# Kernel tuning notes

Measured on AMD Instinct MI355X. Metric: run time of the kernel, lower is better.

## Reference

```python
import jax, jax.numpy as jnp
import numpy as np

B, C, H, HEADS, WS, TOPK = 16, 112, 64, 4, 4, 128
NWH = H // WS          # 16 windows per side
NWIN = NWH * NWH       # 256 windows
HD = C // HEADS        # 28
SCALE = HD ** -0.5


def _topk_indices():
    # Geometric top-K closest full-res pixels per window center (level 0 of focal attention).
    f = H // NWH  # window stride on full-res grid
    qh = np.arange(NWH) * f + f // 2
    cq = np.stack(np.meshgrid(qh, qh, indexing='ij'), 0).reshape(2, -1)            # (2, NWIN)
    ck = np.stack(np.meshgrid(np.arange(H), np.arange(H), indexing='ij'), 0).reshape(2, -1)  # (2, H*H)
    d = np.sqrt(((cq[:, :, None].astype(np.float32) - ck[:, None, :]) ** 2).sum(0))
    return np.argsort(d, axis=1, kind='stable')[:, :TOPK].astype(np.int32)        # (NWIN, TOPK)


def setup_inputs() -> dict:
    key = jax.random.key(0)
    k1, k2, k3 = jax.random.split(key, 3)
    return {
        'x': jax.random.normal(k1, (B, C, H, H), jnp.float32),
        'Wqkv': jax.random.normal(k2, (3 * C, C), jnp.float32) * 0.02,
        'Wproj': jax.random.normal(k3, (C, C), jnp.float32) * 0.02,
        'bproj': jnp.zeros((C,), jnp.float32),
        'topk_idx': jnp.asarray(_topk_indices()),
    }


def reference(x, Wqkv, Wproj, bproj, topk_idx):
    Bv, Cv, Hv, Wv = x.shape
    nwin = (Hv // WS) * (Wv // WS)
    xt = jnp.transpose(x, (0, 2, 3, 1))                       # (B, H, W, C)
    qkv = jnp.einsum('bhwc,dc->bhwd', xt, Wqkv)               # 1x1 conv == matmul
    q, k, v = jnp.split(qkv, 3, axis=-1)
    # Window-partition queries: (B*nwin, heads, ws^2, hd)
    qw = q.reshape(Bv, Hv // WS, WS, Wv // WS, WS, Cv)
    qw = jnp.transpose(qw, (0, 1, 3, 2, 4, 5)).reshape(Bv * nwin, WS * WS, HEADS, HD)
    qw = jnp.transpose(qw, (0, 2, 1, 3)) * SCALE
    # Gather top-K K/V tokens per window from the full-resolution token list
    kf = k.reshape(Bv, Hv * Wv, HEADS, HD)
    vf = v.reshape(Bv, Hv * Wv, HEADS, HD)
    ksel = kf[:, topk_idx]                                    # (B, nwin, TOPK, heads, hd)
    vsel = vf[:, topk_idx]
    ksel = jnp.transpose(ksel, (0, 1, 3, 2, 4)).reshape(Bv * nwin, HEADS, TOPK, HD)
    vsel = jnp.transpose(vsel, (0, 1, 3, 2, 4)).reshape(Bv * nwin, HEADS, TOPK, HD)
    # Windowed attention over gathered KV
    attn = jax.nn.softmax(jnp.einsum('whqd,whkd->whqk', qw, ksel), axis=-1)
    o = jnp.einsum('whqk,whkd->whqd', attn, vsel)             # (B*nwin, heads, ws^2, hd)
    o = jnp.transpose(o, (0, 2, 1, 3)).reshape(Bv * nwin, WS * WS, Cv)
    # Window reverse -> (B, H, W, C)
    o = o.reshape(Bv, Hv // WS, Wv // WS, WS, WS, Cv)
    o = jnp.transpose(o, (0, 1, 3, 2, 4, 5)).reshape(Bv, Hv, Wv, Cv)
    out = jnp.einsum('bhwc,dc->bhwd', o, Wproj) + bproj
    return jnp.transpose(out, (0, 3, 1, 2))                   # (B, C, H, W)
```

## Files before the change

### kernel.cpp

```cpp
#include <hip/hip_runtime.h>
#include <hip/hip_bf16.h>
#include <cstdint>

#define B_ 16
#define C_ 112
#define HEADS_ 4
#define HD_ 28
#define NWIN_ 256
#define TOPK_ 128
#define D3_ 336
#define SCALE_ 0.18898223650461363f

typedef __attribute__((ext_vector_type(4))) float f32x4;
typedef __attribute__((ext_vector_type(8))) short short8;
typedef unsigned uint4u __attribute__((ext_vector_type(4), aligned(4)));

union Frag { unsigned u[4]; uint4 u4; short8 s; };

__device__ inline unsigned cvtpk(float a, float b) {
    unsigned r;
    asm("v_cvt_pk_bf16_f32 %0, %1, %2" : "=v"(r) : "v"(a), "v"(b));
    return r;
}
__device__ inline float bflo(unsigned u) { return __uint_as_float(u << 16); }
__device__ inline float bfhi(unsigned u) { return __uint_as_float(u & 0xFFFF0000u); }

__global__ __launch_bounds__(256) void wt_kernel(const float* __restrict__ W, const float* __restrict__ Wp,
                                                 uint4* __restrict__ WAq,
                                                 uint4* __restrict__ WAh, uint4* __restrict__ WAl) {
    const int id = blockIdx.x * 256 + threadIdx.x;
    if (id < 5376) {
        const int ks = id / 1344, rem = id % 1344;
        const int tile = rem >> 6, l = rem & 63;
        const int d = tile * 16 + (l & 15);
        const int cb = ks * 32 + (l >> 4) * 8;
        float v[8];
        #pragma unroll
        for (int j = 0; j < 8; ++j) { int c = cb + j; v[j] = (c < C_) ? W[d * C_ + c] : 0.f; }
        uint4 o;
        o.x = cvtpk(v[0], v[1]); o.y = cvtpk(v[2], v[3]);
        o.z = cvtpk(v[4], v[5]); o.w = cvtpk(v[6], v[7]);
        WAq[id] = o;
    } else if (id < 5376 + 1792) {
        const int id2 = id - 5376;
        const int ks = id2 / 448, rem = id2 % 448;
        const int tile = rem >> 6, l = rem & 63;
        const int d = tile * 16 + (l & 15);
        const int cb = ks * 32 + (l >> 4) * 8;
        float v[8];
        #pragma unroll
        for (int j = 0; j < 8; ++j) { int c = cb + j; v[j] = (c < C_) ? Wp[d * C_ + c] : 0.f; }
        unsigned hw_[4], lw_[4];
        #pragma unroll
        for (int p = 0; p < 4; ++p) {
            unsigned hh = cvtpk(v[2 * p], v[2 * p + 1]);
            hw_[p] = hh;
            lw_[p] = cvtpk(v[2 * p] - bflo(hh), v[2 * p + 1] - bfhi(hh));
        }
        WAh[id2] = make_uint4(hw_[0], hw_[1], hw_[2], hw_[3]);
        WAl[id2] = make_uint4(lw_[0], lw_[1], lw_[2], lw_[3]);
    }
}

__global__ __launch_bounds__(256) void qkv_kernel(const float* __restrict__ x,
                                                  const uint4* __restrict__ WAq,
                                                  ushort* __restrict__ qkv) {
    __shared__ unsigned xs[64][132];
    const int hw0 = blockIdx.x << 7;
    const int dblk = blockIdx.y;
    const int b = blockIdx.z;
    const int tid = threadIdx.x;
    for (int i = tid; i < 2048; i += 256) {
        const int c2 = i >> 5, j4 = (i & 31) << 2;
        uint4 o = make_uint4(0, 0, 0, 0);
        if (c2 < 56) {
            const float* r0 = x + (((size_t)b * C_ + 2 * c2) << 12) + hw0 + j4;
            float4 a = *(const float4*)r0;
            float4 c = *(const float4*)(r0 + 4096);
            o.x = cvtpk(a.x, c.x); o.y = cvtpk(a.y, c.y);
            o.z = cvtpk(a.z, c.z); o.w = cvtpk(a.w, c.w);
        }
        *(uint4*)&xs[c2][j4] = o;
    }
    __syncthreads();
    const int wv = tid >> 6, l = tid & 63, lq = l & 15, g = l >> 4;
    const int hwl = wv << 5;
    f32x4 acc[7][2] = {};
    #pragma unroll
    for (int ks = 0; ks < 4; ++ks) {
        Frag bf[2];
        #pragma unroll
        for (int n = 0; n < 2; ++n) {
            const int col = hwl + (n << 4) + lq;
            const int r0 = (ks << 4) + (g << 2);
            bf[n].u[0] = xs[r0][col]; bf[n].u[1] = xs[r0 + 1][col];
            bf[n].u[2] = xs[r0 + 2][col]; bf[n].u[3] = xs[r0 + 3][col];
        }
        const uint4* wp = WAq + ((ks * 21 + dblk * 7) << 6) + l;
        #pragma unroll
        for (int m = 0; m < 7; ++m) {
            Frag af; af.u4 = wp[m << 6];
            acc[m][0] = __builtin_amdgcn_mfma_f32_16x16x32_bf16(af.s, bf[0].s, acc[m][0], 0, 0, 0);
            acc[m][1] = __builtin_amdgcn_mfma_f32_16x16x32_bf16(af.s, bf[1].s, acc[m][1], 0, 0, 0);
        }
    }
    const size_t hwbase = ((size_t)b << 12) + hw0;
    #pragma unroll
    for (int m = 0; m < 7; ++m) {
        const int d0 = dblk * 112 + (m << 4) + (g << 2);
        #pragma unroll
        for (int n = 0; n < 2; ++n) {
            const int hw = hwl + (n << 4) + lq;
            uint2 o2;
            o2.x = cvtpk(acc[m][n][0], acc[m][n][1]);
            o2.y = cvtpk(acc[m][n][2], acc[m][n][3]);
            *(uint2*)(qkv + (hwbase + hw) * D3_ + d0) = o2;
        }
    }
}

__global__ __launch_bounds__(256) void attn_kernel(const ushort* __restrict__ qkv,
                                                   const int* __restrict__ topk,
                                                   float* __restrict__ obuf) {
    __shared__ int idxs[TOPK_];
    __shared__ __align__(16) unsigned vsT[4][32][68];
    __shared__ __align__(16) unsigned plds[4][16][68];
    const int b = blockIdx.y, w = blockIdx.x;
    const int wy = w >> 4, wx = w & 15;
    const int tid = threadIdx.x;
    const int wv = tid >> 6, l = tid & 63, lq = l & 15, g = l >> 4;
    if (tid < TOPK_) idxs[tid] = topk[w * TOPK_ + tid];
    __syncthreads();
    const int h = wv;
    const size_t bbase = (size_t)(b << 12);
    const int hwq = ((wy * 4 + (lq >> 2)) << 6) + (wx << 2) + (lq & 3);
    Frag qf;
    {
        uint4u t = *(const uint4u*)(qkv + (bbase + hwq) * D3_ + h * HD_ + (g << 3));
        qf.u[0] = t[0]; qf.u[1] = t[1];
        qf.u[2] = (g == 3) ? 0u : t[2];
        qf.u[3] = (g == 3) ? 0u : t[3];
    }
    Frag kf[8];
    #pragma unroll
    for (int m = 0; m < 8; ++m) {
        const int kr = idxs[(m << 4) + lq];
        uint4u t = *(const uint4u*)(qkv + (bbase + kr) * D3_ + C_ + h * HD_ + (g << 3));
        kf[m].u[0] = t[0]; kf[m].u[1] = t[1]; kf[m].u[2] = t[2]; kf[m].u[3] = t[3];
    }
    {
        const ushort* v0 = qkv + (bbase + idxs[2 * l]) * D3_ + 2 * C_ + h * HD_;
        const ushort* v1 = qkv + (bbase + idxs[2 * l + 1]) * D3_ + 2 * C_ + h * HD_;
        unsigned w0[14], w1[14];
        { uint4u a = *(const uint4u*)v0;        w0[0]=a[0]; w0[1]=a[1]; w0[2]=a[2]; w0[3]=a[3]; }
        { uint4u a = *(const uint4u*)(v0 + 8);  w0[4]=a[0]; w0[5]=a[1]; w0[6]=a[2]; w0[7]=a[3]; }
        { uint4u a = *(const uint4u*)(v0 + 16); w0[8]=a[0]; w0[9]=a[1]; w0[10]=a[2]; w0[11]=a[3]; }
        { uint2 a = *(const uint2*)(v0 + 24);   w0[12]=a.x; w0[13]=a.y; }
        { uint4u a = *(const uint4u*)v1;        w1[0]=a[0]; w1[1]=a[1]; w1[2]=a[2]; w1[3]=a[3]; }
        { uint4u a = *(const uint4u*)(v1 + 8);  w1[4]=a[0]; w1[5]=a[1]; w1[6]=a[2]; w1[7]=a[3]; }
        { uint4u a = *(const uint4u*)(v1 + 16); w1[8]=a[0]; w1[9]=a[1]; w1[10]=a[2]; w1[11]=a[3]; }
        { uint2 a = *(const uint2*)(v1 + 24);   w1[12]=a.x; w1[13]=a.y; }
        #pragma unroll
        for (int j = 0; j < 14; ++j) {
            vsT[wv][2 * j][l]     = __builtin_amdgcn_perm(w1[j], w0[j], 0x05040100);
            vsT[wv][2 * j + 1][l] = __builtin_amdgcn_perm(w1[j], w0[j], 0x07060302);
        }
    }
    f32x4 sacc[8];
    #pragma unroll
    for (int m = 0; m < 8; ++m) {
        f32x4 z = {0.f, 0.f, 0.f, 0.f};
        sacc[m] = __builtin_amdgcn_mfma_f32_16x16x32_bf16(kf[m].s, qf.s, z, 0, 0, 0);
    }
    float mx = -1e30f;
    #pragma unroll
    for (int m = 0; m < 8; ++m)
        #pragma unroll
        for (int r = 0; r < 4; ++r) { sacc[m][r] *= SCALE_; mx = fmaxf(mx, sacc[m][r]); }
    mx = fmaxf(mx, __shfl_xor(mx, 16, 64));
    mx = fmaxf(mx, __shfl_xor(mx, 32, 64));
    float sum = 0.f;
    #pragma unroll
    for (int m = 0; m < 8; ++m)
        #pragma unroll
        for (int r = 0; r < 4; ++r) { float e = __expf(sacc[m][r] - mx); sacc[m][r] = e; sum += e; }
    sum += __shfl_xor(sum, 16, 64);
    sum += __shfl_xor(sum, 32, 64);
    const float inv = 1.f / sum;
    #pragma unroll
    for (int m = 0; m < 8; ++m) {
        unsigned u0 = cvtpk(sacc[m][0] * inv, sacc[m][1] * inv);
        unsigned u1 = cvtpk(sacc[m][2] * inv, sacc[m][3] * inv);
        *(uint2*)&plds[wv][lq][(m << 3) + (g << 1)] = make_uint2(u0, u1);
    }
    f32x4 oacc[2] = {};
    #pragma unroll
    for (int ks = 0; ks < 4; ++ks) {
        Frag pb;
        pb.u4 = *(const uint4*)&plds[wv][lq][(g << 2) + (ks << 4)];
        #pragma unroll
        for (int m = 0; m < 2; ++m) {
            Frag va;
            va.u4 = *(const uint4*)&vsT[wv][lq + (m << 4)][(g << 2) + (ks << 4)];
            oacc[m] = __builtin_amdgcn_mfma_f32_16x16x32_bf16(va.s, pb.s, oacc[m], 0, 0, 0);
        }
    }
    #pragma unroll
    for (int m = 0; m < 2; ++m) {
        const int d0 = (g << 2) + (m << 4);
        if (d0 < HD_) {
            #pragma unroll
            for (int r = 0; r < 4; ++r)
                obuf[(((size_t)(b * C_ + h * HD_ + d0 + r)) << 12) + hwq] = oacc[m][r];
        }
    }
}

__global__ __launch_bounds__(256) void proj_kernel(const float* __restrict__ obuf,
                                                   const uint4* __restrict__ WAh,
                                                   const uint4* __restrict__ WAl,
                                                   const float* __restrict__ bp,
                                                   float* __restrict__ out) {
    __shared__ unsigned xh[64][132];
    __shared__ unsigned xl[64][132];
    const int hw0 = blockIdx.x << 7;
    const int b = blockIdx.y;
    const int tid = threadIdx.x;
    for (int i = tid; i < 2048; i += 256) {
        const int c2 = i >> 5, j4 = (i & 31) << 2;
        uint4 oh = make_uint4(0, 0, 0, 0), ol = make_uint4(0, 0, 0, 0);
        if (c2 < 56) {
            const float* r0 = obuf + (((size_t)b * C_ + 2 * c2) << 12) + hw0 + j4;
            float4 a = *(const float4*)r0;
            float4 c = *(const float4*)(r0 + 4096);
            unsigned t;
            t = cvtpk(a.x, c.x); oh.x = t; ol.x = cvtpk(a.x - bflo(t), c.x - bfhi(t));
            t = cvtpk(a.y, c.y); oh.y = t; ol.y = cvtpk(a.y - bflo(t), c.y - bfhi(t));
            t = cvtpk(a.z, c.z); oh.z = t; ol.z = cvtpk(a.z - bflo(t), c.z - bfhi(t));
            t = cvtpk(a.w, c.w); oh.w = t; ol.w = cvtpk(a.w - bflo(t), c.w - bfhi(t));
        }
        *(uint4*)&xh[c2][j4] = oh;
        *(uint4*)&xl[c2][j4] = ol;
    }
    __syncthreads();
    const int wv = tid >> 6, l = tid & 63, lq = l & 15, g = l >> 4;
    const int hwl = wv << 5;
    f32x4 acc[7][2] = {};
    #pragma unroll
    for (int ks = 0; ks < 4; ++ks) {
        Frag bh[2], bl[2];
        #pragma unroll
        for (int n = 0; n < 2; ++n) {
            const int col = hwl + (n << 4) + lq;
            const int r0 = (ks << 4) + (g << 2);
            bh[n].u[0] = xh[r0][col]; bh[n].u[1] = xh[r0 + 1][col];
            bh[n].u[2] = xh[r0 + 2][col]; bh[n].u[3] = xh[r0 + 3][col];
            bl[n].u[0] = xl[r0][col]; bl[n].u[1] = xl[r0 + 1][col];
            bl[n].u[2] = xl[r0 + 2][col]; bl[n].u[3] = xl[r0 + 3][col];
        }
        const uint4* wph = WAh + ((ks * 7) << 6) + l;
        const uint4* wpl = WAl + ((ks * 7) << 6) + l;
        #pragma unroll
        for (int m = 0; m < 7; ++m) {
            Frag ah, al;
            ah.u4 = wph[m << 6];
            al.u4 = wpl[m << 6];
            #pragma unroll
            for (int n = 0; n < 2; ++n) {
                acc[m][n] = __builtin_amdgcn_mfma_f32_16x16x32_bf16(ah.s, bh[n].s, acc[m][n], 0, 0, 0);
                acc[m][n] = __builtin_amdgcn_mfma_f32_16x16x32_bf16(ah.s, bl[n].s, acc[m][n], 0, 0, 0);
                acc[m][n] = __builtin_amdgcn_mfma_f32_16x16x32_bf16(al.s, bh[n].s, acc[m][n], 0, 0, 0);
            }
        }
    }
    #pragma unroll
    for (int m = 0; m < 7; ++m) {
        const int d0 = (m << 4) + (g << 2);
        const float4 bias = *(const float4*)(bp + d0);
        #pragma unroll
        for (int n = 0; n < 2; ++n) {
            const int hw = hw0 + hwl + (n << 4) + lq;
            out[(((size_t)(b * C_ + d0 + 0)) << 12) + hw] = acc[m][n][0] + bias.x;
            out[(((size_t)(b * C_ + d0 + 1)) << 12) + hw] = acc[m][n][1] + bias.y;
            out[(((size_t)(b * C_ + d0 + 2)) << 12) + hw] = acc[m][n][2] + bias.z;
            out[(((size_t)(b * C_ + d0 + 3)) << 12) + hw] = acc[m][n][3] + bias.w;
        }
    }
}

extern "C" void kernel_launch(void* const* d_in, const int* in_sizes, int n_in,
                              void* d_out, int out_size, void* d_ws, size_t ws_size,
                              hipStream_t stream) {
    const float* x     = (const float*)d_in[0];
    const float* Wqkv  = (const float*)d_in[1];
    const float* Wproj = (const float*)d_in[2];
    const float* bproj = (const float*)d_in[3];
    const int*   topk  = (const int*)d_in[4];
    float* out = (float*)d_out;
    char* ws = (char*)d_ws;
    ushort* qkv  = (ushort*)ws;
    float*  obuf = (float*)(ws + 44040192);
    uint4*  WAq  = (uint4*)(ws + 44040192 + 29360128);
    uint4*  WAh  = (uint4*)(ws + 44040192 + 29360128 + 86016);
    uint4*  WAl  = (uint4*)(ws + 44040192 + 29360128 + 86016 + 28672);
    wt_kernel<<<28, 256, 0, stream>>>(Wqkv, Wproj, WAq, WAh, WAl);
    qkv_kernel<<<dim3(32, 3, 16), 256, 0, stream>>>(x, WAq, qkv);
    attn_kernel<<<dim3(NWIN_, 16), 256, 0, stream>>>(qkv, topk, obuf);
    proj_kernel<<<dim3(32, 16), 256, 0, stream>>>(obuf, WAh, WAl, bproj, out);
}
```

Baseline: 165.6 us.

## Fuse output projection into attention kernel via shared-memory staging

Removes the separate proj_kernel and the fp32 obuf round-trip through global memory. Each attention block writes its 16x112 output tile into shared memory, reused from the P buffer, then does the split-bf16 projection with MFMA and writes the final output with bias. In exchange, the attention kernel gains extra syncs and weight loads per window, and only 7 of 8 wave slots do projection work. The output stores become scattered per window (16 pixels across 4 rows) instead of contiguous 128-pixel rows.

```diff
diff --git a/kernel.cpp b/kernel.cpp
--- a/kernel.cpp
+++ b/kernel.cpp
@@ -121,7 +121,10 @@
 
 __global__ __launch_bounds__(256) void attn_kernel(const ushort* __restrict__ qkv,
                                                    const int* __restrict__ topk,
-                                                   float* __restrict__ obuf) {
+                                                   const uint4* __restrict__ WAh,
+                                                   const uint4* __restrict__ WAl,
+                                                   const float* __restrict__ bp,
+                                                   float* __restrict__ out) {
     __shared__ int idxs[TOPK_];
     __shared__ __align__(16) unsigned vsT[4][32][68];
     __shared__ __align__(16) unsigned plds[4][16][68];
@@ -205,85 +208,56 @@
             oacc[m] = __builtin_amdgcn_mfma_f32_16x16x32_bf16(va.s, pb.s, oacc[m], 0, 0, 0);
         }
     }
+    __syncthreads();
+    float* os = (float*)&plds[0][0][0];
+    for (int i = 1904 + tid; i < 2176; i += 256) os[i] = 0.f;
     #pragma unroll
     for (int m = 0; m < 2; ++m) {
         const int d0 = (g << 2) + (m << 4);
         if (d0 < HD_) {
             #pragma unroll
             for (int r = 0; r < 4; ++r)
-                obuf[(((size_t)(b * C_ + h * HD_ + d0 + r)) << 12) + hwq] = oacc[m][r];
-        }
-    }
-}
-
-__global__ __launch_bounds__(256) void proj_kernel(const float* __restrict__ obuf,
-                                                   const uint4* __restrict__ WAh,
-                                                   const uint4* __restrict__ WAl,
-                                                   const float* __restrict__ bp,
-                                                   float* __restrict__ out) {
-    __shared__ unsigned xh[64][132];
-    __shared__ unsigned xl[64][132];
-    const int hw0 = blockIdx.x << 7;
-    const int b = blockIdx.y;
-    const int tid = threadIdx.x;
-    for (int i = tid; i < 2048; i += 256) {
-        const int c2 = i >> 5, j4 = (i & 31) << 2;
-        uint4 oh = make_uint4(0, 0, 0, 0), ol = make_uint4(0, 0, 0, 0);
-        if (c2 < 56) {
-            const float* r0 = obuf + (((size_t)b * C_ + 2 * c2) << 12) + hw0 + j4;
-            float4 a = *(const float4*)r0;
-            float4 c = *(const float4*)(r0 + 4096);
-            unsigned t;
-            t = cvtpk(a.x, c.x); oh.x = t; ol.x = cvtpk(a.x - bflo(t), c.x - bfhi(t));
-            t = cvtpk(a.y, c.y); oh.y = t; ol.y = cvtpk(a.y - bflo(t), c.y - bfhi(t));
-            t = cvtpk(a.z, c.z); oh.z = t; ol.z = cvtpk(a.z - bflo(t), c.z - bfhi(t));
-            t = cvtpk(a.w, c.w); oh.w = t; ol.w = cvtpk(a.w - bflo(t), c.w - bfhi(t));
-        }
-        *(uint4*)&xh[c2][j4] = oh;
-        *(uint4*)&xl[c2][j4] = ol;
-    }
-    __syncthreads();
-    const int wv = tid >> 6, l = tid & 63, lq = l & 15, g = l >> 4;
-    const int hwl = wv << 5;
-    f32x4 acc[7][2] = {};
+                os[(h * HD_ + d0 + r) * 17 + lq] = oacc[m][r];
+        }
+    }
+    __syncthreads();
+    f32x4 pacc[2] = {};
     #pragma unroll
     for (int ks = 0; ks < 4; ++ks) {
-        Frag bh[2], bl[2];
-        #pragma unroll
-        for (int n = 0; n < 2; ++n) {
-            const int col = hwl + (n << 4) + lq;
-            const int r0 = (ks << 4) + (g << 2);
-            bh[n].u[0] = xh[r0][col]; bh[n].u[1] = xh[r0 + 1][col];
-            bh[n].u[2] = xh[r0 + 2][col]; bh[n].u[3] = xh[r0 + 3][col];
-            bl[n].u[0] = xl[r0][col]; bl[n].u[1] = xl[r0 + 1][col];
-            bl[n].u[2] = xl[r0 + 2][col]; bl[n].u[3] = xl[r0 + 3][col];
-        }
-        const uint4* wph = WAh + ((ks * 7) << 6) + l;
-        const uint4* wpl = WAl + ((ks * 7) << 6) + l;
-        #pragma unroll
-        for (int m = 0; m < 7; ++m) {
-            Frag ah, al;
-            ah.u4 = wph[m << 6];
-            al.u4 = wpl[m << 6];
-            #pragma unroll
-            for (int n = 0; n < 2; ++n) {
-                acc[m][n] = __builtin_amdgcn_mfma_f32_16x16x32_bf16(ah.s, bh[n].s, acc[m][n], 0, 0, 0);
-                acc[m][n] = __builtin_amdgcn_mfma_f32_16x16x32_bf16(ah.s, bl[n].s, acc[m][n], 0, 0, 0);
-                acc[m][n] = __builtin_amdgcn_mfma_f32_16x16x32_bf16(al.s, bh[n].s, acc[m][n], 0, 0, 0);
+        const int cb = (g << 3) + (ks << 5);
+        float v[8];
+        #pragma unroll
+        for (int j = 0; j < 8; ++j) v[j] = os[(cb + j) * 17 + lq];
+        Frag bh, bl;
+        #pragma unroll
+        for (int p = 0; p < 4; ++p) {
+            unsigned hh = cvtpk(v[2 * p], v[2 * p + 1]);
+            bh.u[p] = hh;
+            bl.u[p] = cvtpk(v[2 * p] - bflo(hh), v[2 * p + 1] - bfhi(hh));
+        }
+        #pragma unroll
+        for (int mi = 0; mi < 2; ++mi) {
+            const int m = (wv << 1) + mi;
+            if (m < 7) {
+                Frag ah, al;
+                ah.u4 = WAh[((ks * 7 + m) << 6) + l];
+                al.u4 = WAl[((ks * 7 + m) << 6) + l];
+                pacc[mi] = __builtin_amdgcn_mfma_f32_16x16x32_bf16(ah.s, bh.s, pacc[mi], 0, 0, 0);
+                pacc[mi] = __builtin_amdgcn_mfma_f32_16x16x32_bf16(ah.s, bl.s, pacc[mi], 0, 0, 0);
+                pacc[mi] = __builtin_amdgcn_mfma_f32_16x16x32_bf16(al.s, bh.s, pacc[mi], 0, 0, 0);
             }
         }
     }
     #pragma unroll
-    for (int m = 0; m < 7; ++m) {
-        const int d0 = (m << 4) + (g << 2);
-        const float4 bias = *(const float4*)(bp + d0);
-        #pragma unroll
-        for (int n = 0; n < 2; ++n) {
-            const int hw = hw0 + hwl + (n << 4) + lq;
-            out[(((size_t)(b * C_ + d0 + 0)) << 12) + hw] = acc[m][n][0] + bias.x;
-            out[(((size_t)(b * C_ + d0 + 1)) << 12) + hw] = acc[m][n][1] + bias.y;
-            out[(((size_t)(b * C_ + d0 + 2)) << 12) + hw] = acc[m][n][2] + bias.z;
-            out[(((size_t)(b * C_ + d0 + 3)) << 12) + hw] = acc[m][n][3] + bias.w;
+    for (int mi = 0; mi < 2; ++mi) {
+        const int m = (wv << 1) + mi;
+        if (m < 7) {
+            const int d0 = (m << 4) + (g << 2);
+            const float4 bias = *(const float4*)(bp + d0);
+            out[(((size_t)(b * C_ + d0 + 0)) << 12) + hwq] = pacc[mi][0] + bias.x;
+            out[(((size_t)(b * C_ + d0 + 1)) << 12) + hwq] = pacc[mi][1] + bias.y;
+            out[(((size_t)(b * C_ + d0 + 2)) << 12) + hwq] = pacc[mi][2] + bias.z;
+            out[(((size_t)(b * C_ + d0 + 3)) << 12) + hwq] = pacc[mi][3] + bias.w;
         }
     }
 }
@@ -298,13 +272,11 @@
     const int*   topk  = (const int*)d_in[4];
     float* out = (float*)d_out;
     char* ws = (char*)d_ws;
-    ushort* qkv  = (ushort*)ws;
-    float*  obuf = (float*)(ws + 44040192);
-    uint4*  WAq  = (uint4*)(ws + 44040192 + 29360128);
-    uint4*  WAh  = (uint4*)(ws + 44040192 + 29360128 + 86016);
-    uint4*  WAl  = (uint4*)(ws + 44040192 + 29360128 + 86016 + 28672);
+    ushort* qkv = (ushort*)ws;
+    uint4*  WAq = (uint4*)(ws + 44040192);
+    uint4*  WAh = (uint4*)(ws + 44040192 + 86016);
+    uint4*  WAl = (uint4*)(ws + 44040192 + 86016 + 28672);
     wt_kernel<<<28, 256, 0, stream>>>(Wqkv, Wproj, WAq, WAh, WAl);
     qkv_kernel<<<dim3(32, 3, 16), 256, 0, stream>>>(x, WAq, qkv);
-    attn_kernel<<<dim3(NWIN_, 16), 256, 0, stream>>>(qkv, topk, obuf);
-    proj_kernel<<<dim3(32, 16), 256, 0, stream>>>(obuf, WAh, WAl, bproj, out);
-}
+    attn_kernel<<<dim3(NWIN_, 16), 256, 0, stream>>>(qkv, topk, WAh, WAl, bproj, out);
+}
```

Measured after the change: 155.6 us. -6.1%, faster.
